# Optimization experiments

Measured on AMD Instinct MI355X. Metric: run time of the kernel, lower is better.

Reference implementation:

```python
import jax, jax.numpy as jnp
import numpy as np

B, C, H, W = 8, 128, 128, 128
HEADS = 8
EPS = 1e-12  # torch F.normalize default eps


def _dwconv(x, w, pad):
    # x: [B, G, H, W], w: [G, 1, k, k] depthwise kernel
    return jax.lax.conv_general_dilated(
        x, w, window_strides=(1, 1), padding=((pad, pad), (pad, pad)),
        feature_group_count=w.shape[0],
        dimension_numbers=('NCHW', 'OIHW', 'NCHW'))


def setup_inputs() -> dict:
    key = jax.random.key(0)
    ks = jax.random.split(key, 10)
    s = 0.05
    return {
        'x': jax.random.normal(ks[0], (B, C, H, W), jnp.float32),
        'w_qkv': jax.random.normal(ks[1], (3 * C, C), jnp.float32) * s,
        'w_dw3': jax.random.normal(ks[2], (3 * C, 1, 3, 3), jnp.float32) * s,
        'w_dw5': jax.random.normal(ks[3], (3 * C, 1, 5, 5), jnp.float32) * s,
        'w_dw7': jax.random.normal(ks[4], (3 * C, 1, 7, 7), jnp.float32) * s,
        'w_q': jax.random.normal(ks[5], (C, 3 * C), jnp.float32) * s,
        'w_k': jax.random.normal(ks[6], (C, 3 * C), jnp.float32) * s,
        'w_v': jax.random.normal(ks[7], (C, 3 * C), jnp.float32) * s,
        'w_out': jax.random.normal(ks[8], (C, C), jnp.float32) * s,
        'temperature': jnp.ones((HEADS, 1, 1), jnp.float32),
    }


def reference(x, w_qkv, w_dw3, w_dw5, w_dw7, w_q, w_k, w_v, w_out, temperature):
    b, c, h, w = x.shape
    heads = temperature.shape[0]
    # 1x1 qkv conv: [b, 3c, h, w]
    xq = jnp.einsum('bchw,oc->bohw', x, w_qkv)
    # multi-scale depthwise convs on the same qkv tensor
    q1, k1, v1 = jnp.split(_dwconv(xq, w_dw3, 1), 3, axis=1)
    q2, k2, v2 = jnp.split(_dwconv(xq, w_dw5, 2), 3, axis=1)
    q3, k3, v3 = jnp.split(_dwconv(xq, w_dw7, 3), 3, axis=1)
    q = jnp.einsum('bchw,oc->bohw', jnp.concatenate([q1, q2, q3], 1), w_q)
    k = jnp.einsum('bchw,oc->bohw', jnp.concatenate([k1, k2, k3], 1), w_k)
    v = jnp.einsum('bchw,oc->bohw', jnp.concatenate([v1, v2, v3], 1), w_v)
    # [b, head, c_head, h*w]
    dh = c // heads
    q = q.reshape(b, heads, dh, h * w)
    k = k.reshape(b, heads, dh, h * w)
    v = v.reshape(b, heads, dh, h * w)
    # L2 normalize along spatial dim
    q = q / jnp.maximum(jnp.linalg.norm(q, axis=-1, keepdims=True), EPS)
    k = k / jnp.maximum(jnp.linalg.norm(k, axis=-1, keepdims=True), EPS)
    # channel attention: [b, head, c_head, c_head]
    attn = jnp.einsum('bhcn,bhdn->bhcd', q, k) * temperature
    attn = jax.nn.softmax(attn, axis=-1)
    out = jnp.einsum('bhcd,bhdn->bhcn', attn, v).reshape(b, c, h, w)
    return jnp.einsum('bchw,oc->bohw', out, w_out)
```

## Files before the change

### kernel.cpp

```cpp
#include <hip/hip_runtime.h>
#include <hip/hip_bf16.h>

#define NB 8
#define NSP 16384

typedef unsigned short u16;
typedef __attribute__((ext_vector_type(8))) short short8_;
typedef __attribute__((ext_vector_type(8))) unsigned short u16x8;
typedef __attribute__((ext_vector_type(4))) float f32x4;
typedef __attribute__((ext_vector_type(4))) unsigned u32x4;

__device__ __forceinline__ float b2f(u16 u) {
  unsigned v = ((unsigned)u) << 16;
  float f;
  __builtin_memcpy(&f, &v, 4);
  return f;
}
__device__ __forceinline__ u16 f2b(float f) {
  __hip_bfloat16 h = __float2bfloat16(f);
  u16 u;
  __builtin_memcpy(&u, &h, 2);
  return u;
}
__device__ __forceinline__ float ldf(const void* p, size_t i, int isbf) {
  return isbf ? b2f(((const u16*)p)[i]) : ((const float*)p)[i];
}

__global__ __launch_bounds__(256) void prep_all(
    const void* __restrict__ wq, const void* __restrict__ wk,
    const void* __restrict__ wqkv, const void* __restrict__ wv,
    const void* __restrict__ wdw3, const void* __restrict__ wdw5,
    const void* __restrict__ wdw7, const void* __restrict__ temp,
    u16* __restrict__ Wqf, u16* __restrict__ Wkf, u16* __restrict__ Wkvf,
    u16* __restrict__ Wbv, float* __restrict__ Wdww,
    int* __restrict__ flag, float* __restrict__ Sz)
{
  const int isbf = (((const u16*)temp)[0] != 0) ? 1 : 0;
  const int bx = blockIdx.x;
  const int tid = threadIdx.x;

  if (bx < 72) {
    int i = bx * 256 + tid;
    if (i == 0) *flag = isbf;
    if (i < 18432) Sz[i] = 0.f;
  } else if (bx < 144) {
    const int mb = bx - 72;
    const int mat = mb / 24;
    const int fi = (mb - mat * 24) * 256 + tid;
    const int lane = fi & 63, m = (fi >> 6) & 7, ks = (fi >> 9) & 3, blk = fi >> 11;
    const int quad = lane >> 4, col = lane & 15;
    const void* src;
    u16* dst;
    size_t so;
    if (mat == 2) {
      so = (size_t)(blk * 128 + m * 16 + col) * 128 + ks * 32 + quad * 8;
      src = wqkv; dst = Wkvf;
    } else {
      so = (size_t)(m * 16 + col) * 384 + blk * 128 + ks * 32 + quad * 8;
      src = mat ? wk : wq; dst = mat ? Wkf : Wqf;
    }
    if (isbf) {
      *(u16x8*)&dst[(size_t)fi * 8] = *(const u16x8*)((const u16*)src + so);
    } else {
      f32x4 a = *(const f32x4*)((const float*)src + so);
      f32x4 b = *(const f32x4*)((const float*)src + so + 4);
      u16 us[8];
#pragma unroll
      for (int j = 0; j < 4; j++) { us[j] = f2b(a[j]); us[4 + j] = f2b(b[j]); }
      *(u16x8*)&dst[(size_t)fi * 8] = *(u16x8*)us;
    }
  } else if (bx < 336) {
    int i = (bx - 144) * 256 + tid;
    Wbv[i] = isbf ? ((const u16*)wv)[i] : f2b(((const float*)wv)[i]);
  } else {
    int i = (bx - 336) * 256 + tid;
    if (i >= 32256) return;
    int gc = i / 84, t = i - gc * 84;
    float v = 0.f;
    if (t < 9)       v = ldf(wdw3, (size_t)gc * 9 + t, isbf);
    else if (t < 34) v = ldf(wdw5, (size_t)gc * 25 + (t - 9), isbf);
    else if (t < 83) v = ldf(wdw7, (size_t)gc * 49 + (t - 34), isbf);
    Wdww[i] = v;
  }
}

__global__ __launch_bounds__(256) void gemm_mfma(
    const u16* __restrict__ Wb,
    const void* __restrict__ X,
    u16* __restrict__ C, long c_bstride, int M,
    const int* __restrict__ flagp)
{
  const int isbf = *flagp;
  __shared__ u16 Xs[128 * 76];
  __shared__ u16 Cs[128 * 72];
  const int b = blockIdx.z;
  const int n0 = blockIdx.x * 64;
  const int tid = threadIdx.x;
  const size_t xbase = (size_t)b * 2097152 + n0;

  if (isbf) {
    const u16* Xp = (const u16*)X;
#pragma unroll
    for (int i = 0; i < 4; i++) {
      int s = i * 256 + tid;
      int kk = s >> 3, p = (s & 7) * 8;
      u32x4 v = *(const u32x4*)(Xp + xbase + (size_t)kk * NSP + p);
      uint2 lo; lo.x = v[0]; lo.y = v[1];
      uint2 hi; hi.x = v[2]; hi.y = v[3];
      *(uint2*)&Xs[kk * 76 + p]     = lo;
      *(uint2*)&Xs[kk * 76 + p + 4] = hi;
    }
  } else {
    const float* Xp = (const float*)X;
#pragma unroll
    for (int i = 0; i < 4; i++) {
      int s = i * 256 + tid;
      int kk = s >> 3, p = (s & 7) * 8;
      f32x4 fa = *(const f32x4*)(Xp + xbase + (size_t)kk * NSP + p);
      f32x4 fb = *(const f32x4*)(Xp + xbase + (size_t)kk * NSP + p + 4);
      u16 u8v[8];
#pragma unroll
      for (int j = 0; j < 4; j++) u8v[j] = f2b(fa[j]);
#pragma unroll
      for (int j = 0; j < 4; j++) u8v[4 + j] = f2b(fb[j]);
      *(uint2*)&Xs[kk * 76 + p]     = *(uint2*)&u8v[0];
      *(uint2*)&Xs[kk * 76 + p + 4] = *(uint2*)&u8v[4];
    }
  }
  __syncthreads();

  const int wid = tid >> 6, lane = tid & 63;
  const int quad = lane >> 4, col = lane & 15;
  const int nw = wid * 16;
  u16* Cb = C + (size_t)b * c_bstride + n0;
  const short8_* Af = (const short8_*)Wb;

  for (int ob = 0; ob < M; ob += 128) {
    const int obi = ob >> 7;
    f32x4 z = {0.f, 0.f, 0.f, 0.f};
    f32x4 acc[8];
#pragma unroll
    for (int m = 0; m < 8; m++) acc[m] = z;

#pragma unroll
    for (int ks = 0; ks < 4; ks++) {
      const int k0 = ks * 32;
      short8_ bfrag;
#pragma unroll
      for (int j = 0; j < 8; j++)
        bfrag[j] = (short)Xs[(k0 + quad * 8 + j) * 76 + nw + col];
#pragma unroll
      for (int m = 0; m < 8; m++) {
        short8_ afrag = Af[(size_t)(((obi * 4 + ks) * 8 + m) * 64 + lane)];
        acc[m] = __builtin_amdgcn_mfma_f32_16x16x32_bf16(afrag, bfrag, acc[m], 0, 0, 0);
      }
    }

    if (ob) __syncthreads();
#pragma unroll
    for (int m = 0; m < 8; m++)
#pragma unroll
      for (int r = 0; r < 4; r++)
        Cs[(m * 16 + quad * 4 + r) * 72 + nw + col] = f2b(acc[m][r]);
    __syncthreads();
#pragma unroll
    for (int i = 0; i < 4; i++) {
      int u = i * 256 + tid;
      int row = u >> 3, off = (u & 7) * 8;
      u16x8 v = *(const u16x8*)&Cs[row * 72 + off];
      *(u16x8*)(Cb + (size_t)(ob + row) * NSP + off) = v;
    }
  }
}

__global__ __launch_bounds__(256) void convgemm(
    const u16* __restrict__ xqg, long x_bstride, long x_gstride, int gc_base0,
    const float* __restrict__ Wdww,
    const u16* __restrict__ Afrag, long a_bstride, long a_gstride,
    void* __restrict__ Out, long out_gstride, int om,
    const int* __restrict__ flagp)
{
  const int isbf = *flagp;
  __shared__ u16 regA[7680];
  __shared__ float dww[2688];
  u16* in_s = regA;
  u16* Bp = regA;
  const int b = blockIdx.z, g = blockIdx.y;
  const int t0 = blockIdx.x;
  const int t = ((t0 & 7) << 5) | (t0 >> 3);
  const int y0 = (t >> 3) * 4, x0 = (t & 7) * 16;
  const u16* xb = xqg + (size_t)b * x_bstride + (size_t)g * x_gstride;
  const short8_* Af = (const short8_*)(Afrag + (size_t)b * a_bstride + (size_t)g * a_gstride);
  const int gc_base = gc_base0 + g * 128;
  const int tid = threadIdx.x;
  const int cc_t = tid >> 3;
  const int py_t = (tid >> 1) & 3;
  const int xh   = tid & 1;
  const int wid = tid >> 6, lane = tid & 63;
  const int quad = lane >> 4, col = lane & 15;

  const int hy  = lane / 6;
  const int hc4 = lane - hy * 6;
  const int gy_s = y0 - 3 + hy, gx_s = x0 - 4 + hc4 * 4;
  const bool sval = (lane < 60);
  const bool gok = sval && ((unsigned)gy_s < 128u) && ((unsigned)gx_s <= 124u);
  const u16* gsrc0 = xb + (size_t)wid * NSP + (gy_s * 128 + gx_s);
  const int ldso = wid * 240 + hy * 24 + hc4 * 4;

  uint2 hreg[8];

#pragma unroll
  for (int i = 0; i < 8; i++) {
    uint2 v; v.x = 0u; v.y = 0u;
    if (gok) v = *(const uint2*)(gsrc0 + (size_t)(i * 4) * NSP);
    hreg[i] = v;
  }

  f32x4 z = {0.f, 0.f, 0.f, 0.f};
  f32x4 acc[8];
#pragma unroll
  for (int m = 0; m < 8; m++) acc[m] = z;

  for (int chn = 0; chn < 4; chn++) {
    const int c0 = chn * 32;
    if (chn) __syncthreads();

    if (sval) {
#pragma unroll
      for (int i = 0; i < 8; i++)
        *(uint2*)&in_s[ldso + i * 960] = hreg[i];
    }
    {
      const float* wg = Wdww + (size_t)(gc_base + c0) * 84;
#pragma unroll
      for (int i = 0; i < 3; i++) {
        int s = i * 256 + tid;
        if (s < 672) *(f32x4*)&dww[s * 4] = *(const f32x4*)(wg + s * 4);
      }
    }
    __syncthreads();

    if (chn < 3) {
      const u16* gsrc = gsrc0 + (size_t)(c0 + 32) * NSP;
#pragma unroll
      for (int i = 0; i < 8; i++) {
        uint2 v; v.x = 0u; v.y = 0u;
        if (gok) v = *(const uint2*)(gsrc + (size_t)(i * 4) * NSP);
        hreg[i] = v;
      }
    }

    float a0[8], a1[8], a2[8];
#pragma unroll
    for (int px = 0; px < 8; px++) { a0[px] = 0.f; a1[px] = 0.f; a2[px] = 0.f; }
    {
      const float* dwc = dww + cc_t * 84;
      const u16* rowbase = in_s + cc_t * 240 + xh * 8;
#pragma unroll
      for (int dy = 0; dy < 7; dy++) {
        const u16* rp = rowbase + (py_t + dy) * 24;
        u32x4 ra = *(const u32x4*)rp;
        u32x4 rb = *(const u32x4*)(rp + 8);
        float row[14];
#pragma unroll
        for (int j = 0; j < 14; j++) {
          int l = j + 1;
          unsigned wd = (l < 8) ? ra[l >> 1] : rb[(l >> 1) - 4];
          unsigned bits = (l & 1) ? (wd & 0xffff0000u) : (wd << 16);
          __builtin_memcpy(&row[j], &bits, 4);
        }
#pragma unroll
        for (int dx = 0; dx < 7; dx++) {
          float wv = dwc[34 + dy * 7 + dx];
#pragma unroll
          for (int px = 0; px < 8; px++) a2[px] += row[px + dx] * wv;
        }
        if (dy >= 1 && dy <= 5) {
          int dy5 = dy - 1;
#pragma unroll
          for (int dx = 0; dx < 5; dx++) {
            float wv = dwc[9 + dy5 * 5 + dx];
#pragma unroll
            for (int px = 0; px < 8; px++) a1[px] += row[px + 1 + dx] * wv;
          }
        }
        if (dy >= 2 && dy <= 4) {
          int dy3 = dy - 2;
#pragma unroll
          for (int dx = 0; dx < 3; dx++) {
            float wv = dwc[dy3 * 3 + dx];
#pragma unroll
            for (int px = 0; px < 8; px++) a0[px] += row[px + 2 + dx] * wv;
          }
        }
      }
    }
    __syncthreads();

    {
      const int pb = py_t * 16 + xh * 8;
      u16 us[8];
#pragma unroll
      for (int px = 0; px < 8; px++) us[px] = f2b(a0[px]);
      *(uint2*)&Bp[(0 * 32 + cc_t) * 68 + pb]     = *(uint2*)&us[0];
      *(uint2*)&Bp[(0 * 32 + cc_t) * 68 + pb + 4] = *(uint2*)&us[4];
#pragma unroll
      for (int px = 0; px < 8; px++) us[px] = f2b(a1[px]);
      *(uint2*)&Bp[(1 * 32 + cc_t) * 68 + pb]     = *(uint2*)&us[0];
      *(uint2*)&Bp[(1 * 32 + cc_t) * 68 + pb + 4] = *(uint2*)&us[4];
#pragma unroll
      for (int px = 0; px < 8; px++) us[px] = f2b(a2[px]);
      *(uint2*)&Bp[(2 * 32 + cc_t) * 68 + pb]     = *(uint2*)&us[0];
      *(uint2*)&Bp[(2 * 32 + cc_t) * 68 + pb + 4] = *(uint2*)&us[4];
    }
    __syncthreads();

#pragma unroll
    for (int s = 0; s < 3; s++) {
      const int k0 = s * 32;
      short8_ bfrag;
#pragma unroll
      for (int j = 0; j < 8; j++)
        bfrag[j] = (short)Bp[(k0 + quad * 8 + j) * 68 + wid * 16 + col];
#pragma unroll
      for (int m = 0; m < 8; m++) {
        short8_ afrag = Af[(size_t)(((s * 4 + chn) * 8 + m) * 64 + lane)];
        acc[m] = __builtin_amdgcn_mfma_f32_16x16x32_bf16(afrag, bfrag, acc[m], 0, 0, 0);
      }
    }
  }

#pragma unroll
  for (int m = 0; m < 8; m++)
#pragma unroll
    for (int r = 0; r < 4; r++) {
      int o = m * 16 + quad * 4 + r;
      int ng = (y0 + wid) * 128 + x0 + col;
      size_t base = ((size_t)b * 128 + o) * NSP + ng;
      if (om && !isbf) ((float*)Out)[base] = acc[m][r];
      else ((u16*)Out + (size_t)g * out_gstride)[base] = f2b(acc[m][r]);
    }
}

__global__ __launch_bounds__(256) void s_mfma(
    const u16* __restrict__ qb, const u16* __restrict__ kb,
    float* __restrict__ S, float* __restrict__ qs, float* __restrict__ ks)
{
  __shared__ u16 Qs[16 * 520];
  __shared__ u16 Ks[16 * 520];
  const int chunk = blockIdx.x, h = blockIdx.y, b = blockIdx.z;
  const int tid = threadIdx.x;
  const int n0 = chunk * 512;
  const size_t gbase = ((size_t)b * 128 + h * 16) * NSP + n0;

#pragma unroll
  for (int i = 0; i < 4; i++) {
    int idx = i * 256 + tid;
    int row = idx >> 6, off = (idx & 63) * 8;
    *(u16x8*)&Qs[row * 520 + off] = *(const u16x8*)(qb + gbase + (size_t)row * NSP + off);
    *(u16x8*)&Ks[row * 520 + off] = *(const u16x8*)(kb + gbase + (size_t)row * NSP + off);
  }
  __syncthreads();

  const int wid = tid >> 6, lane = tid & 63;
  const int quad = lane >> 4, col = lane & 15;
  const int nb = wid * 128;
  f32x4 acc = {0.f, 0.f, 0.f, 0.f};
  float sq = 0.f, sk = 0.f;
#pragma unroll
  for (int k2 = 0; k2 < 4; k2++) {
    int off = nb + k2 * 32 + quad * 8;
    short8_ qf = *(const short8_*)&Qs[col * 520 + off];
    short8_ kf = *(const short8_*)&Ks[col * 520 + off];
#pragma unroll
    for (int j = 0; j < 8; j++) {
      float qv = b2f((u16)qf[j]), kv = b2f((u16)kf[j]);
      sq += qv * qv; sk += kv * kv;
    }
    acc = __builtin_amdgcn_mfma_f32_16x16x32_bf16(qf, kf, acc, 0, 0, 0);
  }

  sq += __shfl_xor(sq, 16); sq += __shfl_xor(sq, 32);
  sk += __shfl_xor(sk, 16); sk += __shfl_xor(sk, 32);
  if (quad == 0) {
    atomicAdd(&qs[b * 128 + h * 16 + col], sq);
    atomicAdd(&ks[b * 128 + h * 16 + col], sk);
  }

  __syncthreads();
  float* Sred = (float*)Qs;
#pragma unroll
  for (int r = 0; r < 4; r++)
    Sred[wid * 256 + (quad * 4 + r) * 16 + col] = acc[r];
  __syncthreads();
  {
    float v = Sred[tid] + Sred[256 + tid] + Sred[512 + tid] + Sred[768 + tid];
    atomicAdd(&S[((size_t)(b * 8 + h) << 8) + tid], v);
  }
}

__global__ __launch_bounds__(256) void fold_wv(
    const u16* __restrict__ Mmat, const u16* __restrict__ Wbv,
    u16* __restrict__ Wmv)
{
  const int b = blockIdx.y, jb = blockIdx.x;
  const u16* Mb = Mmat + (size_t)b * 16384;
  const int t = threadIdx.x;
  const int o = t >> 1, jh = t & 1;
  const int j0 = jb * 32 + jh * 16;
  float acc[16];
#pragma unroll
  for (int jj = 0; jj < 16; jj++) acc[jj] = 0.f;
  for (int d = 0; d < 128; d++) {
    float mv = b2f(Mb[o * 128 + d]);
    const u16* wr = Wbv + (size_t)d * 384 + j0;
#pragma unroll
    for (int jj = 0; jj < 16; jj++) acc[jj] += mv * b2f(wr[jj]);
  }
  const int kc = j0 >> 7, ks = (j0 >> 5) & 3, q0 = (j0 >> 3) & 3;
  const int m = o >> 4, col = o & 15;
  u16* outb = Wmv + (size_t)b * 49152;
  const int fi0 = ((kc * 4 + ks) * 8 + m) * 64 + q0 * 16 + col;
  u16x8 v8;
#pragma unroll
  for (int jj = 0; jj < 8; jj++) v8[jj] = f2b(acc[jj]);
  *(u16x8*)&outb[(size_t)fi0 * 8] = v8;
#pragma unroll
  for (int jj = 0; jj < 8; jj++) v8[jj] = f2b(acc[8 + jj]);
  *(u16x8*)&outb[(size_t)(fi0 + 16) * 8] = v8;
}

__global__ __launch_bounds__(256) void attn_mat(
    const float* __restrict__ S, const float* __restrict__ qs,
    const float* __restrict__ ks,
    const void* __restrict__ w_out, const void* __restrict__ temp,
    u16* __restrict__ Mmat, const int* __restrict__ flagp)
{
  const int isbf = *flagp;
  const int b = blockIdx.x;
  __shared__ float attn_s[8 * 16 * 16];
  const int t = threadIdx.x;
  if (t < 128) {
    int h = t >> 4, c = t & 15;
    float qn = fmaxf(sqrtf(fmaxf(qs[b * 128 + h * 16 + c], 0.f)), 1e-12f);
    float tm = ldf(temp, h, isbf);
    float zv[16];
    float m = -1e30f;
    for (int d = 0; d < 16; d++) {
      float kn = fmaxf(sqrtf(fmaxf(ks[b * 128 + h * 16 + d], 0.f)), 1e-12f);
      zv[d] = S[(((size_t)b * 8 + h) * 16 + c) * 16 + d] / (qn * kn) * tm;
      m = fmaxf(m, zv[d]);
    }
    float sum = 0.f;
    for (int d = 0; d < 16; d++) { zv[d] = expf(zv[d] - m); sum += zv[d]; }
    float inv = 1.f / sum;
    for (int d = 0; d < 16; d++) attn_s[(h * 16 + c) * 16 + d] = zv[d] * inv;
  }
  __syncthreads();
  for (int idx = t; idx < 128 * 128; idx += 256) {
    int o = idx >> 7, cp = idx & 127;
    int h = cp >> 4, e = cp & 15;
    float a = 0.f;
    for (int d = 0; d < 16; d++)
      a += ldf(w_out, (size_t)o * 128 + h * 16 + d, isbf) * attn_s[(h * 16 + d) * 16 + e];
    Mmat[(size_t)b * 16384 + idx] = f2b(a);
  }
}

extern "C" void kernel_launch(void* const* d_in, const int* in_sizes, int n_in,
                              void* d_out, int out_size, void* d_ws, size_t ws_size,
                              hipStream_t stream) {
  const void* x     = d_in[0];
  const void* w_qkv = d_in[1];
  const void* w_dw3 = d_in[2];
  const void* w_dw5 = d_in[3];
  const void* w_dw7 = d_in[4];
  const void* w_q   = d_in[5];
  const void* w_k   = d_in[6];
  const void* w_v   = d_in[7];
  const void* w_o   = d_in[8];
  const void* temp  = d_in[9];

  char* ws = (char*)d_ws;
  u16* dsc = (u16*)d_out;
  u16* Wbqf  = dsc;
  u16* Wbkf  = dsc + 49152;
  u16* Wbkvf = dsc + 98304;

  u16* xq    = (u16*)ws;
  u16* q     = (u16*)(ws + 100663296);
  char* tail = ws + 167772160;
  float* S   = (float*)tail;
  float* qs  = (float*)(tail + 65536);
  float* ks  = (float*)(tail + 69632);
  int* flag  = (int*)(tail + 73728);
  u16* Mmat  = (u16*)(tail + 73856);
  u16* Wbv   = (u16*)(tail + 336000);
  u16* Wmv   = (u16*)(tail + 434304);
  float* Wdww = (float*)(tail + 1220736);
  u16* k     = q + 16777216;

  prep_all<<<462, 256, 0, stream>>>(
      w_q, w_k, w_qkv, w_v, w_dw3, w_dw5, w_dw7, temp,
      Wbqf, Wbkf, Wbkvf, Wbv, Wdww, flag, S);

  gemm_mfma<<<dim3(256, 1, NB), 256, 0, stream>>>(
      Wbkvf, x, xq, 384L * NSP, 384, flag);

  convgemm<<<dim3(256, 2, NB), 256, 0, stream>>>(
      xq, 384L * NSP, 128L * NSP, 0, Wdww,
      Wbqf, 0, 49152, q, 16777216L, 0, flag);

  s_mfma<<<dim3(32, 8, NB), 256, 0, stream>>>(q, k, S, qs, ks);

  attn_mat<<<NB, 256, 0, stream>>>(S, qs, ks, w_o, temp, Mmat, flag);
  fold_wv<<<dim3(12, NB), 256, 0, stream>>>(Mmat, Wbv, Wmv);

  convgemm<<<dim3(256, 1, NB), 256, 0, stream>>>(
      xq + 256L * NSP, 384L * NSP, 0, 256, Wdww,
      Wmv, 49152, 0, d_out, 0, 1, flag);
}
```

Baseline: 479.5 us.

## Split conv input and GEMM operand LDS buffers and prefetch weights into registers

Gives the depthwise-conv input tile and the GEMM B operand separate shared-memory buffers instead of aliasing them. Depthwise weights for the next channel chunk are prefetched into registers and stored to LDS together with the next input tile, during the MFMA phase. This removes two barriers per chunk and overlaps the LDS refill with the matrix work. The cost is more LDS per block, which may lower occupancy, and extra registers for the prefetched weights.

```diff
diff --git a/kernel.cpp b/kernel.cpp
--- a/kernel.cpp
+++ b/kernel.cpp
@@ -181,10 +181,9 @@
     const int* __restrict__ flagp)
 {
   const int isbf = *flagp;
-  __shared__ u16 regA[7680];
+  __shared__ u16 in_s[32 * 240];
   __shared__ float dww[2688];
-  u16* in_s = regA;
-  u16* Bp = regA;
+  __shared__ u16 Bp[96 * 68];
   const int b = blockIdx.z, g = blockIdx.y;
   const int t0 = blockIdx.x;
   const int t = ((t0 & 7) << 5) | (t0 >> 3);
@@ -208,6 +207,7 @@
   const int ldso = wid * 240 + hy * 24 + hc4 * 4;
 
   uint2 hreg[8];
+  f32x4 wreg[3];
 
 #pragma unroll
   for (int i = 0; i < 8; i++) {
@@ -215,6 +215,26 @@
     if (gok) v = *(const uint2*)(gsrc0 + (size_t)(i * 4) * NSP);
     hreg[i] = v;
   }
+  {
+    const float* wg = Wdww + (size_t)gc_base * 84;
+#pragma unroll
+    for (int i = 0; i < 3; i++) {
+      int s = i * 256 + tid;
+      f32x4 wv = {0.f, 0.f, 0.f, 0.f};
+      if (s < 672) wv = *(const f32x4*)(wg + s * 4);
+      wreg[i] = wv;
+    }
+  }
+  if (sval) {
+#pragma unroll
+    for (int i = 0; i < 8; i++)
+      *(uint2*)&in_s[ldso + i * 960] = hreg[i];
+  }
+#pragma unroll
+  for (int i = 0; i < 3; i++) {
+    int s = i * 256 + tid;
+    if (s < 672) *(f32x4*)&dww[s * 4] = wreg[i];
+  }
 
   f32x4 z = {0.f, 0.f, 0.f, 0.f};
   f32x4 acc[8];
@@ -223,21 +243,6 @@
 
   for (int chn = 0; chn < 4; chn++) {
     const int c0 = chn * 32;
-    if (chn) __syncthreads();
-
-    if (sval) {
-#pragma unroll
-      for (int i = 0; i < 8; i++)
-        *(uint2*)&in_s[ldso + i * 960] = hreg[i];
-    }
-    {
-      const float* wg = Wdww + (size_t)(gc_base + c0) * 84;
-#pragma unroll
-      for (int i = 0; i < 3; i++) {
-        int s = i * 256 + tid;
-        if (s < 672) *(f32x4*)&dww[s * 4] = *(const f32x4*)(wg + s * 4);
-      }
-    }
     __syncthreads();
 
     if (chn < 3) {
@@ -247,6 +252,14 @@
         uint2 v; v.x = 0u; v.y = 0u;
         if (gok) v = *(const uint2*)(gsrc + (size_t)(i * 4) * NSP);
         hreg[i] = v;
+      }
+      const float* wg = Wdww + (size_t)(gc_base + c0 + 32) * 84;
+#pragma unroll
+      for (int i = 0; i < 3; i++) {
+        int s = i * 256 + tid;
+        f32x4 wv = {0.f, 0.f, 0.f, 0.f};
+        if (s < 672) wv = *(const f32x4*)(wg + s * 4);
+        wreg[i] = wv;
       }
     }
 
@@ -295,7 +308,6 @@
         }
       }
     }
-    __syncthreads();
 
     {
       const int pb = py_t * 16 + xh * 8;
@@ -314,6 +326,19 @@
       *(uint2*)&Bp[(2 * 32 + cc_t) * 68 + pb + 4] = *(uint2*)&us[4];
     }
     __syncthreads();
+
+    if (chn < 3) {
+      if (sval) {
+#pragma unroll
+        for (int i = 0; i < 8; i++)
+          *(uint2*)&in_s[ldso + i * 960] = hreg[i];
+      }
+#pragma unroll
+      for (int i = 0; i < 3; i++) {
+        int s = i * 256 + tid;
+        if (s < 672) *(f32x4*)&dww[s * 4] = wreg[i];
+      }
+    }
 
 #pragma unroll
     for (int s = 0; s < 3; s++) {
```

New measurement: 473.9 us, median of 2. Within noise of the previous version (-1.2%).
